# Optimization experiments

Hardware: AMD Instinct MI355X
Metric: run time of the kernel (lower is better)

## Reference

```python
import jax, jax.numpy as jnp
import numpy as np

N = 8192      # number of nodes
D = 256       # embedding dim
K = 32        # k_degree
EPS = 1e-6


def setup_inputs() -> dict:
    key = jax.random.key(0)
    k1, k2 = jax.random.split(key)
    x = jax.random.normal(k1, (N, D), dtype=jnp.float32)
    q = jax.random.uniform(k2, (N, N), dtype=jnp.float32)  # gumbel uniform noise
    temperature = jnp.array([0.001], dtype=jnp.float32)    # learned nn.Parameter
    return {"x": x, "q": q, "temperature": temperature}


def reference(x, q, temperature):
    # torch: dist_mat = sum(x - x.unsqueeze(1), dim=-1) ** 2
    # dist_mat[i, j] = (sum_f x[j,f] - sum_f x[i,f])^2 = (s[j] - s[i])^2
    s = jnp.sum(x, axis=-1)                      # [N]
    dist_mat = (s[None, :] - s[:, None]) ** 2    # [N, N]
    probs = jnp.exp(-temperature[0] * dist_mat) + EPS

    # Gumbel-perturbed logits, top-k per column via argsort along axis 0
    g = jnp.log(probs + EPS) - jnp.log(-jnp.log(q + EPS))  # [N, N]
    child_nodes = jnp.argsort(g, axis=0)[-K:].reshape(-1)   # [K*N]
    parent_nodes = jnp.tile(jnp.arange(N, dtype=child_nodes.dtype), K)  # [K*N]

    # symmetric scatter of adjacency mask
    mask = jnp.zeros((N, N), dtype=x.dtype)
    mask = mask.at[child_nodes, parent_nodes].set(1.0)
    mask = mask.at[parent_nodes, child_nodes].set(1.0)

    edge_index = jnp.stack([child_nodes, parent_nodes])      # [2, K*N]
    edge_weights = jnp.ones((edge_index.shape[1],), dtype=x.dtype)
    return edge_index, edge_weights, probs, mask, dist_mat
```

## Files before the change

kernel.cpp:

```cpp
#include <hip/hip_runtime.h>
#include <stdint.h>

typedef unsigned long long ull;
typedef float __attribute__((ext_vector_type(4))) floatx4;
#define NN 8192
#define KK 32

__device__ __forceinline__ ull make_key(float g, uint32_t idx) {
    uint32_t b = __float_as_uint(g);
    uint32_t k = b ^ (0x80000000u | (uint32_t)((int32_t)b >> 31));
    return ((ull)k << 32) | idx;
}

__device__ __forceinline__ void cas_both(ull &a, ull &b) {
    ull x = a, y = b;
    bool g = x < y;
    a = g ? y : x;
    b = g ? x : y;
}

__device__ __forceinline__ void sort16_desc(ull (&c)[16]) {
#pragma unroll
    for (int k = 2; k <= 16; k <<= 1) {
#pragma unroll
        for (int j = k >> 1; j > 0; j >>= 1) {
#pragma unroll
            for (int i = 0; i < 16; ++i) {
                int l = i ^ j;
                if (l > i) {
                    if ((i & k) == 0) cas_both(c[i], c[l]);
                    else              cas_both(c[l], c[i]);
                }
            }
        }
    }
}

__device__ __forceinline__ void bmerge32_desc(ull (&c)[32]) {
#pragma unroll
    for (int j = 16; j > 0; j >>= 1) {
#pragma unroll
        for (int i = 0; i < 32; ++i) {
            if ((i & j) == 0) cas_both(c[i], c[i ^ j]);
        }
    }
}

__device__ __forceinline__ void merge_into32(ull (&acc)[32], const ull (&ch)[32]) {
#pragma unroll
    for (int k = 0; k < 32; ++k) {
        ull a = acc[31 - k], b = ch[k];
        acc[31 - k] = a >= b ? a : b;
    }
    bmerge32_desc(acc);
}

__device__ __forceinline__ void load_list32(const ull* __restrict__ src, int list,
                                            int j, ull (&ch)[32]) {
#pragma unroll
    for (int k = 0; k < 32; ++k)
        ch[k] = src[((size_t)list * 32 + k) * NN + j];
}

__global__ __launch_bounds__(256) void k_rowsum(const float* __restrict__ x,
                                                float* __restrict__ s) {
    int row  = blockIdx.x * 4 + (threadIdx.x >> 6);
    int lane = threadIdx.x & 63;
    float4 v = reinterpret_cast<const float4*>(x)[(size_t)row * 64 + lane];
    float sum = (v.x + v.y) + (v.z + v.w);
#pragma unroll
    for (int off = 1; off < 64; off <<= 1) sum += __shfl_xor(sum, off, 64);
    if (lane == 0) s[row] = sum;
}

__global__ __launch_bounds__(256, 4) void k_fused(const float* __restrict__ q,
                                                  const float* __restrict__ s,
                                                  const float* __restrict__ tptr,
                                                  float* __restrict__ dist_out,
                                                  float* __restrict__ probs_out,
                                                  float* __restrict__ mask,
                                                  ull* __restrict__ cand,
                                                  int segr, int nthreads) {
    const uint32_t j = blockIdx.x * 256 + threadIdx.x;
    const uint32_t gtid =
        (blockIdx.y * (NN / 256) + blockIdx.x) * 256 + threadIdx.x;
    const float sj = s[j];
    const float temp = tptr[0];

    ull top[32];
#pragma unroll
    for (int k = 0; k < 32; ++k) top[k] = 0;

    const uint32_t i0 = (uint32_t)blockIdx.y * (uint32_t)segr;
    for (uint32_t r = 0; r < (uint32_t)segr; r += 16) {
        const uint32_t it = r >> 4;
        const uint32_t ib = i0 + r;
        const uint32_t off0 = ib * NN + j;

        ull ch[16];
        {
            float qv[8];
#pragma unroll
            for (uint32_t u = 0; u < 8; ++u) qv[u] = q[off0 + u * NN];
#pragma unroll
            for (uint32_t u = 0; u < 8; ++u) {
                float diff = sj - s[ib + u];
                float d = diff * diff;
                float pr = expf(-(temp * d)) + 1e-6f;
                uint32_t off = off0 + u * NN;
                __builtin_nontemporal_store(d, &dist_out[off]);
                __builtin_nontemporal_store(pr, &probs_out[off]);
                float a = logf(pr + 1e-6f);
                float b = logf(-logf(qv[u] + 1e-6f));
                ch[u] = make_key(a - b, ib + u);
            }
        }
        {
            float qv[8];
#pragma unroll
            for (uint32_t u = 0; u < 8; ++u) qv[u] = q[off0 + (8 + u) * NN];
#pragma unroll
            for (uint32_t u = 0; u < 8; ++u) {
                float diff = sj - s[ib + 8 + u];
                float d = diff * diff;
                float pr = expf(-(temp * d)) + 1e-6f;
                uint32_t off = off0 + (8 + u) * NN;
                __builtin_nontemporal_store(d, &dist_out[off]);
                __builtin_nontemporal_store(pr, &probs_out[off]);
                float a = logf(pr + 1e-6f);
                float b = logf(-logf(qv[u] + 1e-6f));
                ch[8 + u] = make_key(a - b, ib + 8 + u);
            }
        }
        {
            floatx4* mask4 = (floatx4*)mask;
            const floatx4 z4 = {0.f, 0.f, 0.f, 0.f};
#pragma unroll
            for (uint32_t u = 0; u < 4; ++u)
                __builtin_nontemporal_store(
                    z4, &mask4[(it * 4 + u) * (uint32_t)nthreads + gtid]);
        }

        sort16_desc(ch);
#pragma unroll
        for (int u = 0; u < 16; ++u) {
            ull a = top[16 + u], b = ch[15 - u];
            top[16 + u] = a >= b ? a : b;
        }
        bmerge32_desc(top);
    }
    const uint32_t base = (uint32_t)blockIdx.y * (KK * NN) + j;
#pragma unroll
    for (uint32_t k = 0; k < KK; ++k) cand[base + k * NN] = top[k];
}

__global__ __launch_bounds__(256) void k_merge1(const ull* __restrict__ src,
                                                ull* __restrict__ dst,
                                                int lists_per_grp) {
    int gid = blockIdx.x * 256 + threadIdx.x;
    int j   = gid & (NN - 1);
    int grp = gid >> 13;
    ull acc[32];
    load_list32(src, grp * lists_per_grp, j, acc);
    for (int l = 1; l < lists_per_grp; ++l) {
        ull ch[32];
        load_list32(src, grp * lists_per_grp + l, j, ch);
        merge_into32(acc, ch);
    }
    const size_t base = (size_t)grp * KK * NN + j;
#pragma unroll
    for (int k = 0; k < KK; ++k) dst[base + (size_t)k * NN] = acc[k];
}

__global__ __launch_bounds__(64) void k_final(const ull* __restrict__ src,
                                              float* __restrict__ out) {
    const int j = blockIdx.x * 64 + threadIdx.x;
    ull acc[32];
    load_list32(src, 0, j, acc);
#pragma unroll
    for (int l = 1; l < 4; ++l) {
        ull ch[32];
        load_list32(src, l, j, ch);
        merge_into32(acc, ch);
    }
    const size_t KN = (size_t)KK * NN;
    float* child  = out;
    float* parent = out + KN;
    float* wts    = out + 2 * KN;
#pragma unroll
    for (int k = 0; k < KK; ++k) {
        uint32_t c = (uint32_t)acc[KK - 1 - k];
        child [(size_t)k * NN + j] = (float)c;
        parent[(size_t)k * NN + j] = (float)j;
        wts   [(size_t)k * NN + j] = 1.0f;
    }
}

__global__ __launch_bounds__(256) void k_scatter(const float* __restrict__ child,
                                                 float* __restrict__ mask) {
    int gid = blockIdx.x * 256 + threadIdx.x;
    int j = gid & (NN - 1);
    int k = gid >> 13;
    uint32_t c = (uint32_t)child[(size_t)k * NN + j];
    mask[(size_t)c * NN + j] = 1.0f;
    mask[(size_t)j * NN + c] = 1.0f;
}

extern "C" void kernel_launch(void* const* d_in, const int* in_sizes, int n_in,
                              void* d_out, int out_size, void* d_ws, size_t ws_size,
                              hipStream_t stream) {
    const float* x    = (const float*)d_in[0];
    const float* q    = (const float*)d_in[1];
    const float* tptr = (const float*)d_in[2];
    float* out = (float*)d_out;

    const size_t KN = (size_t)KK * NN;
    float* probs_out = out + 3 * KN;
    float* mask_out  = out + 3 * KN + (size_t)NN * NN;
    float* dist_out  = out + 3 * KN + 2 * (size_t)NN * NN;

    const size_t cand1_bytes = (size_t)NN * 4 * KK * 8;
    int nseg = 32;
    if (ws_size < 65536 + (size_t)NN * 32 * KK * 8 + cand1_bytes) nseg = 16;
    const int segr = NN / nseg;
    const int nthreads = (NN / 256) * nseg * 256;
    float* s = (float*)d_ws;
    ull* cand0 = (ull*)((char*)d_ws + 65536);
    ull* cand1 = cand0 + (size_t)NN * nseg * KK;

    k_rowsum<<<NN / 4, 256, 0, stream>>>(x, s);
    k_fused<<<dim3(NN / 256, nseg), 256, 0, stream>>>(
        q, s, tptr, dist_out, probs_out, mask_out, cand0, segr, nthreads);
    k_merge1<<<(NN * 4) / 256, 256, 0, stream>>>(cand0, cand1, nseg / 4);
    k_final<<<NN / 64, 64, 0, stream>>>(cand1, out);
    k_scatter<<<(KK * NN) / 256, 256, 0, stream>>>(out, mask_out);
}
```

Baseline: 329.3 us.

## Split fused kernel into streaming output writer and top-k selection kernel

Un-fuses the main kernel. A new vectorized streaming kernel writes dist, probs and the zeroed mask with 16-byte nontemporal stores. A separate selection kernel reads q with nontemporal loads and does only the Gumbel top-k, writing candidates nontemporally. The goal is to separate the bandwidth-bound writes from the compute and register-heavy sort so that each runs at its own best efficiency. The cost is recomputing dist and probs in both kernels plus one extra launch.

```diff
diff --git a/kernel.cpp b/kernel.cpp
--- a/kernel.cpp
+++ b/kernel.cpp
@@ -73,17 +73,38 @@
     if (lane == 0) s[row] = sum;
 }
 
-__global__ __launch_bounds__(256, 4) void k_fused(const float* __restrict__ q,
-                                                  const float* __restrict__ s,
-                                                  const float* __restrict__ tptr,
-                                                  float* __restrict__ dist_out,
-                                                  float* __restrict__ probs_out,
-                                                  float* __restrict__ mask,
-                                                  ull* __restrict__ cand,
-                                                  int segr, int nthreads) {
+__global__ __launch_bounds__(256) void k_streams(const float* __restrict__ s,
+                                                 const float* __restrict__ tptr,
+                                                 floatx4* __restrict__ dist4,
+                                                 floatx4* __restrict__ probs4,
+                                                 floatx4* __restrict__ mask4) {
+    const uint32_t gid = blockIdx.x * 256 + threadIdx.x;
+    const uint32_t i = gid >> 11;
+    const uint32_t j4 = gid & 2047;
+    const float si = s[i];
+    const floatx4 sj = ((const floatx4*)s)[j4];
+    const float temp = tptr[0];
+
+    floatx4 d, pr;
+#pragma unroll
+    for (int u = 0; u < 4; ++u) {
+        float diff = sj[u] - si;
+        float dd = diff * diff;
+        d[u]  = dd;
+        pr[u] = expf(-(temp * dd)) + 1e-6f;
+    }
+    const floatx4 z4 = {0.f, 0.f, 0.f, 0.f};
+    __builtin_nontemporal_store(d,  &dist4[gid]);
+    __builtin_nontemporal_store(pr, &probs4[gid]);
+    __builtin_nontemporal_store(z4, &mask4[gid]);
+}
+
+__global__ __launch_bounds__(256, 4) void k_select(const float* __restrict__ q,
+                                                   const float* __restrict__ s,
+                                                   const float* __restrict__ tptr,
+                                                   ull* __restrict__ cand,
+                                                   int segr) {
     const uint32_t j = blockIdx.x * 256 + threadIdx.x;
-    const uint32_t gtid =
-        (blockIdx.y * (NN / 256) + blockIdx.x) * 256 + threadIdx.x;
     const float sj = s[j];
     const float temp = tptr[0];
 
@@ -93,7 +114,6 @@
 
     const uint32_t i0 = (uint32_t)blockIdx.y * (uint32_t)segr;
     for (uint32_t r = 0; r < (uint32_t)segr; r += 16) {
-        const uint32_t it = r >> 4;
         const uint32_t ib = i0 + r;
         const uint32_t off0 = ib * NN + j;
 
@@ -101,15 +121,13 @@
         {
             float qv[8];
 #pragma unroll
-            for (uint32_t u = 0; u < 8; ++u) qv[u] = q[off0 + u * NN];
+            for (uint32_t u = 0; u < 8; ++u)
+                qv[u] = __builtin_nontemporal_load(&q[off0 + u * NN]);
 #pragma unroll
             for (uint32_t u = 0; u < 8; ++u) {
                 float diff = sj - s[ib + u];
                 float d = diff * diff;
                 float pr = expf(-(temp * d)) + 1e-6f;
-                uint32_t off = off0 + u * NN;
-                __builtin_nontemporal_store(d, &dist_out[off]);
-                __builtin_nontemporal_store(pr, &probs_out[off]);
                 float a = logf(pr + 1e-6f);
                 float b = logf(-logf(qv[u] + 1e-6f));
                 ch[u] = make_key(a - b, ib + u);
@@ -118,28 +136,18 @@
         {
             float qv[8];
 #pragma unroll
-            for (uint32_t u = 0; u < 8; ++u) qv[u] = q[off0 + (8 + u) * NN];
+            for (uint32_t u = 0; u < 8; ++u)
+                qv[u] = __builtin_nontemporal_load(&q[off0 + (8 + u) * NN]);
 #pragma unroll
             for (uint32_t u = 0; u < 8; ++u) {
                 float diff = sj - s[ib + 8 + u];
                 float d = diff * diff;
                 float pr = expf(-(temp * d)) + 1e-6f;
-                uint32_t off = off0 + (8 + u) * NN;
-                __builtin_nontemporal_store(d, &dist_out[off]);
-                __builtin_nontemporal_store(pr, &probs_out[off]);
                 float a = logf(pr + 1e-6f);
                 float b = logf(-logf(qv[u] + 1e-6f));
                 ch[8 + u] = make_key(a - b, ib + 8 + u);
             }
         }
-        {
-            floatx4* mask4 = (floatx4*)mask;
-            const floatx4 z4 = {0.f, 0.f, 0.f, 0.f};
-#pragma unroll
-            for (uint32_t u = 0; u < 4; ++u)
-                __builtin_nontemporal_store(
-                    z4, &mask4[(it * 4 + u) * (uint32_t)nthreads + gtid]);
-        }
 
         sort16_desc(ch);
 #pragma unroll
@@ -151,7 +159,8 @@
     }
     const uint32_t base = (uint32_t)blockIdx.y * (KK * NN) + j;
 #pragma unroll
-    for (uint32_t k = 0; k < KK; ++k) cand[base + k * NN] = top[k];
+    for (uint32_t k = 0; k < KK; ++k)
+        __builtin_nontemporal_store(top[k], &cand[base + k * NN]);
 }
 
 __global__ __launch_bounds__(256) void k_merge1(const ull* __restrict__ src,
@@ -223,14 +232,14 @@
     int nseg = 32;
     if (ws_size < 65536 + (size_t)NN * 32 * KK * 8 + cand1_bytes) nseg = 16;
     const int segr = NN / nseg;
-    const int nthreads = (NN / 256) * nseg * 256;
     float* s = (float*)d_ws;
     ull* cand0 = (ull*)((char*)d_ws + 65536);
     ull* cand1 = cand0 + (size_t)NN * nseg * KK;
 
     k_rowsum<<<NN / 4, 256, 0, stream>>>(x, s);
-    k_fused<<<dim3(NN / 256, nseg), 256, 0, stream>>>(
-        q, s, tptr, dist_out, probs_out, mask_out, cand0, segr, nthreads);
+    k_streams<<<(NN * (NN / 4)) / 256, 256, 0, stream>>>(
+        s, tptr, (floatx4*)dist_out, (floatx4*)probs_out, (floatx4*)mask_out);
+    k_select<<<dim3(NN / 256, nseg), 256, 0, stream>>>(q, s, tptr, cand0, segr);
     k_merge1<<<(NN * 4) / 256, 256, 0, stream>>>(cand0, cand1, nseg / 4);
     k_final<<<NN / 64, 64, 0, stream>>>(cand1, out);
     k_scatter<<<(KK * NN) / 256, 256, 0, stream>>>(out, mask_out);
```

Result: slower. 435.5 us (+32.3%).

## Split fused kernel into interleaved compute-topk and streaming-store block roles

Applied to the files above, without the earlier changes.

The single fused kernel becomes a heterogeneous kernel in which most blocks only read q and compute the top-k candidates, while every period-th block streams the dist, probs and mask-zero outputs with vectorized nontemporal stores. The goal is to separate the compute-bound top-k work from the write-bandwidth-bound output stores so they run side by side on different CUs, and to widen the output stores to 16 bytes. In exchange, dist and probs are computed twice (once in the top-k blocks without storing, once in the store blocks), and the balance depends on the period ratio and on block scheduling order.

```diff
diff --git a/kernel.cpp b/kernel.cpp
--- a/kernel.cpp
+++ b/kernel.cpp
@@ -73,85 +73,103 @@
     if (lane == 0) s[row] = sum;
 }
 
-__global__ __launch_bounds__(256, 4) void k_fused(const float* __restrict__ q,
-                                                  const float* __restrict__ s,
-                                                  const float* __restrict__ tptr,
-                                                  float* __restrict__ dist_out,
-                                                  float* __restrict__ probs_out,
-                                                  float* __restrict__ mask,
-                                                  ull* __restrict__ cand,
-                                                  int segr, int nthreads) {
-    const uint32_t j = blockIdx.x * 256 + threadIdx.x;
-    const uint32_t gtid =
-        (blockIdx.y * (NN / 256) + blockIdx.x) * 256 + threadIdx.x;
-    const float sj = s[j];
+__global__ __launch_bounds__(256, 4) void k_mega(const float* __restrict__ q,
+                                                 const float* __restrict__ s,
+                                                 const float* __restrict__ tptr,
+                                                 float* __restrict__ dist_out,
+                                                 float* __restrict__ probs_out,
+                                                 float* __restrict__ mask,
+                                                 ull* __restrict__ cand,
+                                                 int segr, int period) {
+    const uint32_t b = blockIdx.x;
+    const uint32_t tid = threadIdx.x;
     const float temp = tptr[0];
-
-    ull top[32];
-#pragma unroll
-    for (int k = 0; k < 32; ++k) top[k] = 0;
-
-    const uint32_t i0 = (uint32_t)blockIdx.y * (uint32_t)segr;
-    for (uint32_t r = 0; r < (uint32_t)segr; r += 16) {
-        const uint32_t it = r >> 4;
-        const uint32_t ib = i0 + r;
-        const uint32_t off0 = ib * NN + j;
-
-        ull ch[16];
-        {
-            float qv[8];
-#pragma unroll
-            for (uint32_t u = 0; u < 8; ++u) qv[u] = q[off0 + u * NN];
-#pragma unroll
-            for (uint32_t u = 0; u < 8; ++u) {
-                float diff = sj - s[ib + u];
-                float d = diff * diff;
-                float pr = expf(-(temp * d)) + 1e-6f;
-                uint32_t off = off0 + u * NN;
-                __builtin_nontemporal_store(d, &dist_out[off]);
-                __builtin_nontemporal_store(pr, &probs_out[off]);
-                float a = logf(pr + 1e-6f);
-                float b = logf(-logf(qv[u] + 1e-6f));
-                ch[u] = make_key(a - b, ib + u);
-            }
-        }
-        {
-            float qv[8];
-#pragma unroll
-            for (uint32_t u = 0; u < 8; ++u) qv[u] = q[off0 + (8 + u) * NN];
-#pragma unroll
-            for (uint32_t u = 0; u < 8; ++u) {
-                float diff = sj - s[ib + 8 + u];
-                float d = diff * diff;
-                float pr = expf(-(temp * d)) + 1e-6f;
-                uint32_t off = off0 + (8 + u) * NN;
-                __builtin_nontemporal_store(d, &dist_out[off]);
-                __builtin_nontemporal_store(pr, &probs_out[off]);
-                float a = logf(pr + 1e-6f);
-                float b = logf(-logf(qv[u] + 1e-6f));
-                ch[8 + u] = make_key(a - b, ib + 8 + u);
-            }
-        }
-        {
-            floatx4* mask4 = (floatx4*)mask;
-            const floatx4 z4 = {0.f, 0.f, 0.f, 0.f};
-#pragma unroll
-            for (uint32_t u = 0; u < 4; ++u)
-                __builtin_nontemporal_store(
-                    z4, &mask4[(it * 4 + u) * (uint32_t)nthreads + gtid]);
-        }
-
-        sort16_desc(ch);
-#pragma unroll
-        for (int u = 0; u < 16; ++u) {
-            ull a = top[16 + u], b = ch[15 - u];
-            top[16 + u] = a >= b ? a : b;
-        }
-        bmerge32_desc(top);
-    }
-    const uint32_t base = (uint32_t)blockIdx.y * (KK * NN) + j;
-#pragma unroll
-    for (uint32_t k = 0; k < KK; ++k) cand[base + k * NN] = top[k];
+    const uint32_t p = (uint32_t)period;
+
+    if ((b % p) != (p - 1)) {
+        const uint32_t sb = b - (b + 1) / p;
+        const uint32_t colblk = sb & 31;
+        const uint32_t seg = sb >> 5;
+        const uint32_t j = colblk * 256 + tid;
+        const float sj = s[j];
+
+        ull top[32];
+#pragma unroll
+        for (int k = 0; k < 32; ++k) top[k] = 0;
+
+        const uint32_t i0 = seg * (uint32_t)segr;
+        for (uint32_t r = 0; r < (uint32_t)segr; r += 16) {
+            const uint32_t ib = i0 + r;
+            const uint32_t off0 = ib * NN + j;
+
+            ull ch[16];
+            {
+                float qv[8];
+#pragma unroll
+                for (uint32_t u = 0; u < 8; ++u) qv[u] = q[off0 + u * NN];
+#pragma unroll
+                for (uint32_t u = 0; u < 8; ++u) {
+                    float diff = sj - s[ib + u];
+                    float d = diff * diff;
+                    float pr = expf(-(temp * d)) + 1e-6f;
+                    float a = logf(pr + 1e-6f);
+                    float bb = logf(-logf(qv[u] + 1e-6f));
+                    ch[u] = make_key(a - bb, ib + u);
+                }
+            }
+            {
+                float qv[8];
+#pragma unroll
+                for (uint32_t u = 0; u < 8; ++u) qv[u] = q[off0 + (8 + u) * NN];
+#pragma unroll
+                for (uint32_t u = 0; u < 8; ++u) {
+                    float diff = sj - s[ib + 8 + u];
+                    float d = diff * diff;
+                    float pr = expf(-(temp * d)) + 1e-6f;
+                    float a = logf(pr + 1e-6f);
+                    float bb = logf(-logf(qv[u] + 1e-6f));
+                    ch[8 + u] = make_key(a - bb, ib + 8 + u);
+                }
+            }
+
+            sort16_desc(ch);
+#pragma unroll
+            for (int u = 0; u < 16; ++u) {
+                ull a = top[16 + u], bb = ch[15 - u];
+                top[16 + u] = a >= bb ? a : bb;
+            }
+            bmerge32_desc(top);
+        }
+        const uint32_t base = seg * (KK * NN) + j;
+#pragma unroll
+        for (uint32_t k = 0; k < KK; ++k) cand[base + k * NN] = top[k];
+    } else {
+        const uint32_t t = ((b + 1) / p - 1) * 256 + tid;
+        floatx4* dist4  = (floatx4*)dist_out;
+        floatx4* probs4 = (floatx4*)probs_out;
+        floatx4* mask4  = (floatx4*)mask;
+        const floatx4* s4 = (const floatx4*)s;
+
+        for (uint32_t k = 0; k < 128; ++k) {
+            uint32_t idx = k * 131072u + t;
+            uint32_t i = idx >> 11, j4 = idx & 2047u;
+            float si = s[i];
+            floatx4 sj = s4[j4];
+            floatx4 d, pr;
+#pragma unroll
+            for (int u = 0; u < 4; ++u) {
+                float diff = sj[u] - si;
+                float dd = diff * diff;
+                d[u]  = dd;
+                pr[u] = expf(-(temp * dd)) + 1e-6f;
+            }
+            __builtin_nontemporal_store(d,  &dist4[idx]);
+            __builtin_nontemporal_store(pr, &probs4[idx]);
+        }
+        const floatx4 z4 = {0.f, 0.f, 0.f, 0.f};
+        for (uint32_t k = 0; k < 128; ++k)
+            __builtin_nontemporal_store(z4, &mask4[k * 131072u + t]);
+    }
 }
 
 __global__ __launch_bounds__(256) void k_merge1(const ull* __restrict__ src,
@@ -220,17 +238,19 @@
     float* dist_out  = out + 3 * KN + 2 * (size_t)NN * NN;
 
     const size_t cand1_bytes = (size_t)NN * 4 * KK * 8;
-    int nseg = 32;
-    if (ws_size < 65536 + (size_t)NN * 32 * KK * 8 + cand1_bytes) nseg = 16;
+    int nseg = 32, period = 3;
+    if (ws_size < 65536 + (size_t)NN * 32 * KK * 8 + cand1_bytes) {
+        nseg = 16; period = 2;
+    }
     const int segr = NN / nseg;
-    const int nthreads = (NN / 256) * nseg * 256;
+    const int grid = nseg * 32 + 512;
     float* s = (float*)d_ws;
     ull* cand0 = (ull*)((char*)d_ws + 65536);
     ull* cand1 = cand0 + (size_t)NN * nseg * KK;
 
     k_rowsum<<<NN / 4, 256, 0, stream>>>(x, s);
-    k_fused<<<dim3(NN / 256, nseg), 256, 0, stream>>>(
-        q, s, tptr, dist_out, probs_out, mask_out, cand0, segr, nthreads);
+    k_mega<<<grid, 256, 0, stream>>>(q, s, tptr, dist_out, probs_out,
+                                     mask_out, cand0, segr, period);
     k_merge1<<<(NN * 4) / 256, 256, 0, stream>>>(cand0, cand1, nseg / 4);
     k_final<<<NN / 64, 64, 0, stream>>>(cand1, out);
     k_scatter<<<(KK * NN) / 256, 256, 0, stream>>>(out, mask_out);
```

Result: slower. 361.2 us (+9.7%).
